# Kernel optimization log

Hardware: AMD Instinct MI355X
Metric: run time of the kernel (lower is better)

## Reference

```python
import jax, jax.numpy as jnp
import numpy as np

EMBED = 1024
HEAD = 64

def setup_inputs() -> dict:
    key = jax.random.key(0)
    k1, k2, k3, k4 = jax.random.split(key, 4)
    x = jax.random.normal(k1, (8, 2048, EMBED), dtype=jnp.float32)
    # nn.Linear(E, H, bias=False) weights, stored as [E, H] for x @ W
    W_k = jax.random.normal(k2, (EMBED, HEAD), dtype=jnp.float32) * (EMBED ** -0.5)
    W_q = jax.random.normal(k3, (EMBED, HEAD), dtype=jnp.float32) * (EMBED ** -0.5)
    W_v = jax.random.normal(k4, (EMBED, HEAD), dtype=jnp.float32) * (EMBED ** -0.5)
    return {"x": x, "W_k": W_k, "W_q": W_q, "W_v": W_v}

def reference(x, W_k, W_q, W_v):
    B, T, E = x.shape
    keys = jnp.einsum('bte,eh->bth', x, W_k)
    queries = jnp.einsum('bte,eh->bth', x, W_q)
    values = jnp.einsum('bte,eh->bth', x, W_v)
    # NOTE: original scales by embedding size E, not head size
    scores = jnp.einsum('bqh,bkh->bqk', queries, keys) * (E ** -0.5)
    causal = jnp.tril(jnp.ones((T, T), dtype=bool))
    scores = jnp.where(causal, scores, -jnp.inf)
    weights = jax.nn.softmax(scores, axis=-1)
    return jnp.einsum('bqk,bkh->bqh', weights, values)
```

## Files before the change

### kernel.cpp

```cpp
#include <hip/hip_runtime.h>

typedef __attribute__((ext_vector_type(8))) short bf16x8;
typedef __attribute__((ext_vector_type(4))) float f32x4;
typedef __attribute__((ext_vector_type(4))) unsigned short u16x4;
typedef __attribute__((ext_vector_type(8))) unsigned short u16x8;
typedef __attribute__((ext_vector_type(4))) unsigned int u32x4;

#define MFMA(a, b, c) __builtin_amdgcn_mfma_f32_16x16x32_bf16(a, b, c, 0, 0, 0)

static __device__ __forceinline__ unsigned short f2bf(float x) {
    union { float f; unsigned u; } v; v.f = x;
    unsigned r = v.u + 0x7fffu + ((v.u >> 16) & 1u);
    return (unsigned short)(r >> 16);
}

static __device__ __forceinline__ bf16x8 pack_pa(
    float ea0, float ea1, float ea2, float ea3,
    float eb0, float eb1, float eb2, float eb3, bool odd)
{
    unsigned a1, a2, b1, b2;
    asm("v_cvt_pk_bf16_f32 %0, %1, %2" : "=v"(a1) : "v"(ea0), "v"(ea1));
    asm("v_cvt_pk_bf16_f32 %0, %1, %2" : "=v"(a2) : "v"(ea2), "v"(ea3));
    asm("v_cvt_pk_bf16_f32 %0, %1, %2" : "=v"(b1) : "v"(eb0), "v"(eb1));
    asm("v_cvt_pk_bf16_f32 %0, %1, %2" : "=v"(b2) : "v"(eb2), "v"(eb3));
    asm("v_permlane32_swap_b32 %0, %1" : "+v"(a1), "+v"(b1));
    asm("v_permlane32_swap_b32 %0, %1" : "+v"(a2), "+v"(b2));
    int sa1 = __shfl_xor((int)a1, 16);
    int sa2 = __shfl_xor((int)a2, 16);
    int sb1 = __shfl_xor((int)b1, 16);
    int sb2 = __shfl_xor((int)b2, 16);
    u32x4 paw;
    paw[0] = odd ? (unsigned)sb1 : a1;
    paw[1] = odd ? (unsigned)sb2 : a2;
    paw[2] = odd ? b1 : (unsigned)sa1;
    paw[3] = odd ? b2 : (unsigned)sa2;
    return __builtin_bit_cast(bf16x8, paw);
}

__global__ __launch_bounds__(256) void wtrans_k(
    const float* __restrict__ Wk, const float* __restrict__ Wq,
    const float* __restrict__ Wv, unsigned short* __restrict__ Wt)
{
    __shared__ float tl[64][65];
    const int w = blockIdx.x >> 4, kt = blockIdx.x & 15;
    const float* W = (w == 0) ? Wk : (w == 1) ? Wq : Wv;
    const int tid = threadIdx.x;
#pragma unroll
    for (int rep = 0; rep < 4; rep++) {
        int flat = rep * 256 + tid;
        int rr = flat >> 4, c4 = (flat & 15) * 4;
        f32x4 v = *(const f32x4*)(W + (kt * 64 + rr) * 64 + c4);
#pragma unroll
        for (int jj = 0; jj < 4; jj++) tl[c4 + jj][rr] = v[jj];
    }
    __syncthreads();
#pragma unroll
    for (int rep = 0; rep < 2; rep++) {
        int flat = rep * 256 + tid;
        int n = flat >> 3, k8 = (flat & 7) * 8;
        u16x8 h;
#pragma unroll
        for (int jj = 0; jj < 8; jj++) h[jj] = f2bf(tl[n][k8 + jj]);
        *(u16x8*)(Wt + w * 65536 + n * 1024 + kt * 64 + k8) = h;
    }
}

__global__ __launch_bounds__(256) void qkv_k(
    const float* __restrict__ x, const unsigned short* __restrict__ Wt,
    unsigned short* __restrict__ Qb, unsigned short* __restrict__ Kb,
    unsigned short* __restrict__ Vt)
{
    __shared__ __align__(16) unsigned short xl[32][72];
    __shared__ __align__(16) unsigned short wl[192][72];
    const int tid = threadIdx.x;
    const int wid = tid >> 6, lane = tid & 63;
    const int lrow = lane & 15, g = lane >> 4;
    const int mbase = blockIdx.x * 32;
    const int msrow = (wid & 1) * 16;
    const int ntbase = (wid >> 1) * 6;

    f32x4 acc[6];
#pragma unroll
    for (int jj = 0; jj < 6; jj++) acc[jj] = (f32x4){0.f, 0.f, 0.f, 0.f};

    for (int kc = 0; kc < 1024; kc += 64) {
#pragma unroll
        for (int rep = 0; rep < 2; rep++) {
            int flat = rep * 256 + tid;
            int row = flat >> 4, c4 = (flat & 15) * 4;
            f32x4 v = *(const f32x4*)(x + (mbase + row) * 1024 + kc + c4);
            unsigned lo, hi;
            asm("v_cvt_pk_bf16_f32 %0, %1, %2" : "=v"(lo) : "v"(v[0]), "v"(v[1]));
            asm("v_cvt_pk_bf16_f32 %0, %1, %2" : "=v"(hi) : "v"(v[2]), "v"(v[3]));
            unsigned* dst = (unsigned*)&xl[row][c4];
            dst[0] = lo; dst[1] = hi;
        }
#pragma unroll
        for (int rep = 0; rep < 6; rep++) {
            int flat = rep * 256 + tid;
            int n = flat >> 3, c = (flat & 7) * 8;
            *(u16x8*)&wl[n][c] = *(const u16x8*)(Wt + n * 1024 + kc + c);
        }
        __syncthreads();
#pragma unroll
        for (int ks = 0; ks < 2; ks++) {
            bf16x8 a = *(const bf16x8*)&xl[msrow + lrow][ks * 32 + g * 8];
#pragma unroll
            for (int jj = 0; jj < 6; jj++) {
                bf16x8 b = *(const bf16x8*)&wl[(ntbase + jj) * 16 + lrow][ks * 32 + g * 8];
                acc[jj] = MFMA(a, b, acc[jj]);
            }
        }
        __syncthreads();
    }

#pragma unroll
    for (int jj = 0; jj < 6; jj++) {
        int nt = ntbase + jj;
        int w = nt >> 2;
        int col = (nt & 3) * 16 + lrow;
        int r0 = mbase + msrow + g * 4;
        if (w == 2) {
            int b = r0 >> 11, t = r0 & 2047;
            u16x4 pv;
            pv[0] = f2bf(acc[jj][0]); pv[1] = f2bf(acc[jj][1]);
            pv[2] = f2bf(acc[jj][2]); pv[3] = f2bf(acc[jj][3]);
            *(u16x4*)(Vt + b * 131072 + col * 2048 + t) = pv;
        } else {
            unsigned short* dst = (w == 0) ? Kb : Qb;
#pragma unroll
            for (int i = 0; i < 4; i++)
                dst[(r0 + i) * 64 + col] = f2bf(acc[jj][i]);
        }
    }
}

__global__ __launch_bounds__(256) void attn_k(
    const unsigned short* __restrict__ Qb, const unsigned short* __restrict__ Kb,
    const unsigned short* __restrict__ Vt, float* __restrict__ pO,
    float* __restrict__ pL)
{
    __shared__ __align__(16) unsigned short klds[2][64][64];
    __shared__ __align__(16) unsigned short vlds[2][64][64];
    const int tid = threadIdx.x;
    const int w = tid >> 6, lane = tid & 63;
    const int lrow = lane & 15, g = lane >> 4;
    const int bid = blockIdx.x;
    const int batch = bid >> 6;
    const int rem = bid & 63;
    const int pi = rem >> 2;
    const int j  = rem & 3;

    const unsigned short* Kbase = Kb + batch * 2048 * 64;
    const unsigned short* Vbase = Vt + batch * 131072;
    const float C2 = 0.03125f * 1.44269504088896f;

    const int sr = tid >> 2;
    const int sc32 = tid & 3;
    const int sb0 = sr * 128 + (((sc32 * 2)     ^ (sr & 7)) << 4);
    const int sb1 = sr * 128 + (((sc32 * 2 + 1) ^ (sr & 7)) << 4);

    const int swz = (lrow & 7) << 4;
    const int rb0 = (lrow) * 128, rb1 = (16 + lrow) * 128,
              rb2 = (32 + lrow) * 128, rb3 = (48 + lrow) * 128;
    const int gk0 = (g << 4) ^ swz;
    const int gk1 = ((4 + g) << 4) ^ swz;
    const bool odd = (g & 1);

#pragma unroll 1
    for (int phase = 0; phase < 2; ++phase) {
        const int B   = phase ? (31 - pi) : pi;
        const int qb  = B * 64;
        const int nch = B + 1;
        const int nc  = (nch > j) ? ((nch - j + 3) >> 2) : 0;

        const unsigned short* Qrow = Qb + (batch * 2048 + qb + w * 16 + lrow) * 64;
        bf16x8 q0 = *(const bf16x8*)(Qrow + g * 8);
        bf16x8 q1 = *(const bf16x8*)(Qrow + 32 + g * 8);
        const int qglob = qb + w * 16 + lrow;

        f32x4 o0 = {0.f,0.f,0.f,0.f}, o1 = o0, o2 = o0, o3 = o0;
        float lsum = 0.f;

        u16x8 rk0 = {}, rk1 = {}, rv0 = {}, rv1 = {};
        if (nc > 0) {
            const int kvb = j * 64;
            const unsigned short* ksrc = Kbase + (kvb + sr) * 64 + sc32 * 16;
            rk0 = *(const u16x8*)(ksrc); rk1 = *(const u16x8*)(ksrc + 8);
            const unsigned short* vsrc = Vbase + sr * 2048 + kvb + sc32 * 16;
            rv0 = *(const u16x8*)(vsrc); rv1 = *(const u16x8*)(vsrc + 8);
            char* kb = (char*)&klds[0][0][0];
            char* vb = (char*)&vlds[0][0][0];
            *(u16x8*)(kb + sb0) = rk0; *(u16x8*)(kb + sb1) = rk1;
            *(u16x8*)(vb + sb0) = rv0; *(u16x8*)(vb + sb1) = rv1;
        }
        __syncthreads();

        for (int idx = 0; idx < nc; ++idx) {
            const int c = j + idx * 4;
            const int cur = idx & 1;
            const int kvbase = c * 64;
            if (idx + 1 < nc) {
                const int kvb = kvbase + 256;
                const unsigned short* ksrc = Kbase + (kvb + sr) * 64 + sc32 * 16;
                rk0 = *(const u16x8*)(ksrc); rk1 = *(const u16x8*)(ksrc + 8);
                const unsigned short* vsrc = Vbase + sr * 2048 + kvb + sc32 * 16;
                rv0 = *(const u16x8*)(vsrc); rv1 = *(const u16x8*)(vsrc + 8);
            }

            const char* kb = (const char*)&klds[cur][0][0];
            const char* vb = (const char*)&vlds[cur][0][0];

            f32x4 t0 = {0.f,0.f,0.f,0.f}, t1 = t0, t2 = t0, t3 = t0;
            {
                bf16x8 a;
                a = *(const bf16x8*)(kb + rb0 + gk0); t0 = MFMA(a, q0, t0);
                a = *(const bf16x8*)(kb + rb0 + gk1); t0 = MFMA(a, q1, t0);
                a = *(const bf16x8*)(kb + rb1 + gk0); t1 = MFMA(a, q0, t1);
                a = *(const bf16x8*)(kb + rb1 + gk1); t1 = MFMA(a, q1, t1);
                a = *(const bf16x8*)(kb + rb2 + gk0); t2 = MFMA(a, q0, t2);
                a = *(const bf16x8*)(kb + rb2 + gk1); t2 = MFMA(a, q1, t2);
                a = *(const bf16x8*)(kb + rb3 + gk0); t3 = MFMA(a, q0, t3);
                a = *(const bf16x8*)(kb + rb3 + gk1); t3 = MFMA(a, q1, t3);
            }

            const bool maskc = (c == nch - 1);
            float eA[4], eB[4], eC[4], eD[4];
#pragma unroll
            for (int u = 0; u < 4; u++) {
                float v0 = t0[u] * C2, v1 = t1[u] * C2,
                      v2 = t2[u] * C2, v3 = t3[u] * C2;
                if (maskc) {
                    int kvr = kvbase + g * 4 + u;
                    v0 = (kvr      > qglob) ? -INFINITY : v0;
                    v1 = (kvr + 16 > qglob) ? -INFINITY : v1;
                    v2 = (kvr + 32 > qglob) ? -INFINITY : v2;
                    v3 = (kvr + 48 > qglob) ? -INFINITY : v3;
                }
                eA[u] = __builtin_exp2f(v0);
                eB[u] = __builtin_exp2f(v1);
                eC[u] = __builtin_exp2f(v2);
                eD[u] = __builtin_exp2f(v3);
                lsum += (eA[u] + eB[u]) + (eC[u] + eD[u]);
            }

            bf16x8 pa0 = pack_pa(eA[0],eA[1],eA[2],eA[3], eB[0],eB[1],eB[2],eB[3], odd);
            bf16x8 pa1 = pack_pa(eC[0],eC[1],eC[2],eC[3], eD[0],eD[1],eD[2],eD[3], odd);

            {
                bf16x8 vv;
                vv = *(const bf16x8*)(vb + rb0 + gk0); o0 = MFMA(pa0, vv, o0);
                vv = *(const bf16x8*)(vb + rb0 + gk1); o0 = MFMA(pa1, vv, o0);
                vv = *(const bf16x8*)(vb + rb1 + gk0); o1 = MFMA(pa0, vv, o1);
                vv = *(const bf16x8*)(vb + rb1 + gk1); o1 = MFMA(pa1, vv, o1);
                vv = *(const bf16x8*)(vb + rb2 + gk0); o2 = MFMA(pa0, vv, o2);
                vv = *(const bf16x8*)(vb + rb2 + gk1); o2 = MFMA(pa1, vv, o2);
                vv = *(const bf16x8*)(vb + rb3 + gk0); o3 = MFMA(pa0, vv, o3);
                vv = *(const bf16x8*)(vb + rb3 + gk1); o3 = MFMA(pa1, vv, o3);
            }

            __syncthreads();
            if (idx + 1 < nc) {
                char* kw = (char*)&klds[cur ^ 1][0][0];
                char* vw = (char*)&vlds[cur ^ 1][0][0];
                *(u16x8*)(kw + sb0) = rk0; *(u16x8*)(kw + sb1) = rk1;
                *(u16x8*)(vw + sb0) = rv0; *(u16x8*)(vw + sb1) = rv1;
            }
            __syncthreads();
        }

        const int qrow0 = batch * 2048 + qb + w * 16;
        float* po = pO + ((size_t)j * 16384 + qrow0) * 64;
#pragma unroll
        for (int u = 0; u < 4; u++) {
            int r = (g * 4 + u) * 64;
            po[r +      lrow] = o0[u];
            po[r + 16 + lrow] = o1[u];
            po[r + 32 + lrow] = o2[u];
            po[r + 48 + lrow] = o3[u];
        }
        lsum += __shfl_xor(lsum, 16);
        lsum += __shfl_xor(lsum, 32);
        if (lane < 16) pL[j * 16384 + qrow0 + lane] = lsum;
        __syncthreads();
    }
}

__global__ __launch_bounds__(256) void comb_k(
    const float* __restrict__ pO, const float* __restrict__ pL,
    float* __restrict__ out)
{
    const int J = 16384 * 64;
    int id = blockIdx.x * 256 + threadIdx.x;
    int row = id >> 2, q = (id & 3) * 16;
    float inv = 1.f / (pL[row] + pL[16384 + row] + pL[32768 + row] + pL[49152 + row]);
    const float* p0 = pO + row * 64 + q;
    float* op = out + row * 64 + q;
#pragma unroll
    for (int k = 0; k < 4; k++) {
        f32x4 s = *(const f32x4*)(p0 + 4 * k)
                + *(const f32x4*)(p0 + J + 4 * k)
                + *(const f32x4*)(p0 + 2 * J + 4 * k)
                + *(const f32x4*)(p0 + 3 * J + 4 * k);
        *(f32x4*)(op + 4 * k) = s * inv;
    }
}

extern "C" void kernel_launch(void* const* d_in, const int* in_sizes, int n_in,
                              void* d_out, int out_size, void* d_ws, size_t ws_size,
                              hipStream_t stream) {
    const float* x  = (const float*)d_in[0];
    const float* Wk = (const float*)d_in[1];
    const float* Wq = (const float*)d_in[2];
    const float* Wv = (const float*)d_in[3];
    float* out = (float*)d_out;

    unsigned short* Wt = (unsigned short*)d_ws;
    unsigned short* Kb = Wt + 3 * 65536;
    unsigned short* Qb = Kb + 16384 * 64;
    unsigned short* Vt = Qb + 16384 * 64;
    float* pO = (float*)(Vt + 131072 * 8);
    float* pL = pO + 4 * 16384 * 64;

    wtrans_k<<<48, 256, 0, stream>>>(Wk, Wq, Wv, Wt);
    qkv_k<<<512, 256, 0, stream>>>(x, Wt, Qb, Kb, Vt);
    attn_k<<<512, 256, 0, stream>>>(Qb, Kb, Vt, pO, pL);
    comb_k<<<256, 256, 0, stream>>>(pO, pL, out);
}
```

Baseline: 53.71 us.

## Double-buffer QKV projection with register prefetch and larger 64-row tiles

Rewrites the QKV projection kernel to prefetch the next K-chunk of x and weights into registers while computing on the current LDS buffer. It uses two LDS buffers so only one barrier per iteration is needed. Block size grows to 512 threads covering 64 rows, which halves the number of blocks and doubles weight reuse per block. The trade-off is more LDS and register use per block, and only 256 blocks, which may underfill the GPU.

```diff
diff --git a/kernel.cpp b/kernel.cpp
--- a/kernel.cpp
+++ b/kernel.cpp
@@ -65,72 +65,93 @@
     }
 }
 
-__global__ __launch_bounds__(256) void qkv_k(
+__global__ __launch_bounds__(512) void qkv_k(
     const float* __restrict__ x, const unsigned short* __restrict__ Wt,
     unsigned short* __restrict__ Qb, unsigned short* __restrict__ Kb,
     unsigned short* __restrict__ Vt)
 {
-    __shared__ __align__(16) unsigned short xl[32][72];
-    __shared__ __align__(16) unsigned short wl[192][72];
+    __shared__ __align__(16) unsigned short xl[2][64][72];
+    __shared__ __align__(16) unsigned short wl[2][192][72];
     const int tid = threadIdx.x;
     const int wid = tid >> 6, lane = tid & 63;
     const int lrow = lane & 15, g = lane >> 4;
-    const int mbase = blockIdx.x * 32;
-    const int msrow = (wid & 1) * 16;
-    const int ntbase = (wid >> 1) * 6;
+    const int mbase = blockIdx.x * 64;
+    const int msrow = (wid & 3) * 16;
+    const int ntbase = (wid >> 2) * 6;
+
+    const int xrow = tid >> 3, xc8 = (tid & 7) * 8;
+    const int wrow = tid >> 3, wc8 = (tid & 7) * 8;
 
     f32x4 acc[6];
 #pragma unroll
-    for (int jj = 0; jj < 6; jj++) acc[jj] = (f32x4){0.f, 0.f, 0.f, 0.f};
-
-    for (int kc = 0; kc < 1024; kc += 64) {
-#pragma unroll
-        for (int rep = 0; rep < 2; rep++) {
-            int flat = rep * 256 + tid;
-            int row = flat >> 4, c4 = (flat & 15) * 4;
-            f32x4 v = *(const f32x4*)(x + (mbase + row) * 1024 + kc + c4);
-            unsigned lo, hi;
-            asm("v_cvt_pk_bf16_f32 %0, %1, %2" : "=v"(lo) : "v"(v[0]), "v"(v[1]));
-            asm("v_cvt_pk_bf16_f32 %0, %1, %2" : "=v"(hi) : "v"(v[2]), "v"(v[3]));
-            unsigned* dst = (unsigned*)&xl[row][c4];
-            dst[0] = lo; dst[1] = hi;
-        }
-#pragma unroll
-        for (int rep = 0; rep < 6; rep++) {
-            int flat = rep * 256 + tid;
-            int n = flat >> 3, c = (flat & 7) * 8;
-            *(u16x8*)&wl[n][c] = *(const u16x8*)(Wt + n * 1024 + kc + c);
+    for (int j = 0; j < 6; j++) acc[j] = (f32x4){0.f, 0.f, 0.f, 0.f};
+
+    f32x4 vx0, vx1;
+    u16x8 rw0, rw1, rw2;
+    {
+        const float* xs = x + (mbase + xrow) * 1024 + xc8;
+        vx0 = *(const f32x4*)(xs);
+        vx1 = *(const f32x4*)(xs + 4);
+        const unsigned short* ws = Wt + wrow * 1024 + wc8;
+        rw0 = *(const u16x8*)(ws);
+        rw1 = *(const u16x8*)(ws + 64 * 1024);
+        rw2 = *(const u16x8*)(ws + 128 * 1024);
+    }
+
+#pragma unroll 1
+    for (int t = 0; t < 16; ++t) {
+        const int buf = t & 1;
+        {
+            unsigned d0, d1, d2, d3;
+            asm("v_cvt_pk_bf16_f32 %0, %1, %2" : "=v"(d0) : "v"(vx0[0]), "v"(vx0[1]));
+            asm("v_cvt_pk_bf16_f32 %0, %1, %2" : "=v"(d1) : "v"(vx0[2]), "v"(vx0[3]));
+            asm("v_cvt_pk_bf16_f32 %0, %1, %2" : "=v"(d2) : "v"(vx1[0]), "v"(vx1[1]));
+            asm("v_cvt_pk_bf16_f32 %0, %1, %2" : "=v"(d3) : "v"(vx1[2]), "v"(vx1[3]));
+            u32x4 pk; pk[0] = d0; pk[1] = d1; pk[2] = d2; pk[3] = d3;
+            *(u32x4*)&xl[buf][xrow][xc8] = pk;
+            *(u16x8*)&wl[buf][wrow][wc8]       = rw0;
+            *(u16x8*)&wl[buf][wrow + 64][wc8]  = rw1;
+            *(u16x8*)&wl[buf][wrow + 128][wc8] = rw2;
+        }
+        if (t < 15) {
+            const int kc = (t + 1) * 64;
+            const float* xs = x + (mbase + xrow) * 1024 + kc + xc8;
+            vx0 = *(const f32x4*)(xs);
+            vx1 = *(const f32x4*)(xs + 4);
+            const unsigned short* ws = Wt + wrow * 1024 + kc + wc8;
+            rw0 = *(const u16x8*)(ws);
+            rw1 = *(const u16x8*)(ws + 64 * 1024);
+            rw2 = *(const u16x8*)(ws + 128 * 1024);
         }
         __syncthreads();
 #pragma unroll
         for (int ks = 0; ks < 2; ks++) {
-            bf16x8 a = *(const bf16x8*)&xl[msrow + lrow][ks * 32 + g * 8];
-#pragma unroll
-            for (int jj = 0; jj < 6; jj++) {
-                bf16x8 b = *(const bf16x8*)&wl[(ntbase + jj) * 16 + lrow][ks * 32 + g * 8];
-                acc[jj] = MFMA(a, b, acc[jj]);
-            }
-        }
-        __syncthreads();
-    }
-
-#pragma unroll
-    for (int jj = 0; jj < 6; jj++) {
-        int nt = ntbase + jj;
+            bf16x8 a = *(const bf16x8*)&xl[buf][msrow + lrow][ks * 32 + g * 8];
+#pragma unroll
+            for (int j = 0; j < 6; j++) {
+                bf16x8 b = *(const bf16x8*)&wl[buf][(ntbase + j) * 16 + lrow][ks * 32 + g * 8];
+                acc[j] = MFMA(a, b, acc[j]);
+            }
+        }
+    }
+
+#pragma unroll
+    for (int j = 0; j < 6; j++) {
+        int nt = ntbase + j;
         int w = nt >> 2;
         int col = (nt & 3) * 16 + lrow;
         int r0 = mbase + msrow + g * 4;
         if (w == 2) {
-            int b = r0 >> 11, t = r0 & 2047;
+            int b = r0 >> 11, tt = r0 & 2047;
             u16x4 pv;
-            pv[0] = f2bf(acc[jj][0]); pv[1] = f2bf(acc[jj][1]);
-            pv[2] = f2bf(acc[jj][2]); pv[3] = f2bf(acc[jj][3]);
-            *(u16x4*)(Vt + b * 131072 + col * 2048 + t) = pv;
+            pv[0] = f2bf(acc[j][0]); pv[1] = f2bf(acc[j][1]);
+            pv[2] = f2bf(acc[j][2]); pv[3] = f2bf(acc[j][3]);
+            *(u16x4*)(Vt + b * 131072 + col * 2048 + tt) = pv;
         } else {
             unsigned short* dst = (w == 0) ? Kb : Qb;
 #pragma unroll
             for (int i = 0; i < 4; i++)
-                dst[(r0 + i) * 64 + col] = f2bf(acc[jj][i]);
+                dst[(r0 + i) * 64 + col] = f2bf(acc[j][i]);
         }
     }
 }
@@ -323,7 +344,7 @@
     float* pL = pO + 4 * 16384 * 64;
 
     wtrans_k<<<48, 256, 0, stream>>>(Wk, Wq, Wv, Wt);
-    qkv_k<<<512, 256, 0, stream>>>(x, Wt, Qb, Kb, Vt);
+    qkv_k<<<256, 512, 0, stream>>>(x, Wt, Qb, Kb, Vt);
     attn_k<<<512, 256, 0, stream>>>(Qb, Kb, Vt, pO, pL);
     comb_k<<<256, 256, 0, stream>>>(pO, pL, out);
 }
```

Result: faster. 49.37 us (-8.1%).
